# Kernel optimization log

Measured on AMD Instinct MI355X. Metric: run time of the kernel, lower is better.

The kernel has to match this reference:

```python
import jax, jax.numpy as jnp
import numpy as np
import math

DIM = 1024
NUM_HEADS = 16
HEAD_DIM = DIM // NUM_HEADS
BLOCK_SIZE = 64


def _block_mask(src_blocks, tgt_blocks, num_blocks):
    # Block-level BigBird mask: global first/last block columns, sliding window of 1, random blocks.
    i = jnp.arange(num_blocks)[:, None]
    j = jnp.arange(num_blocks)[None, :]
    band = jnp.abs(i - j) <= 1
    glob = (j == 0) | (j == num_blocks - 1)
    bm = band | glob
    bm = bm.at[src_blocks, tgt_blocks].set(True)
    return bm  # [nb, nb] bool


def setup_inputs() -> dict:
    key = jax.random.key(0)
    ks = jax.random.split(key, 12)
    B, S = 2, 2048
    x = jax.random.normal(ks[0], (B, S, DIM), dtype=jnp.float32)
    scale = 0.02
    Wq = jax.random.normal(ks[1], (DIM, DIM), dtype=jnp.float32) * scale
    bq = jnp.zeros((DIM,), dtype=jnp.float32)
    Wk = jax.random.normal(ks[2], (DIM, DIM), dtype=jnp.float32) * scale
    bk = jnp.zeros((DIM,), dtype=jnp.float32)
    Wv = jax.random.normal(ks[3], (DIM, DIM), dtype=jnp.float32) * scale
    bv = jnp.zeros((DIM,), dtype=jnp.float32)
    Wo = jax.random.normal(ks[4], (DIM, DIM), dtype=jnp.float32) * scale
    bo = jnp.zeros((DIM,), dtype=jnp.float32)
    num_blocks = S // BLOCK_SIZE
    src_blocks = jax.random.randint(ks[5], (3,), 0, num_blocks, dtype=jnp.int32)
    tgt_blocks = jax.random.randint(ks[6], (3,), 0, num_blocks, dtype=jnp.int32)
    return {"x": x, "Wq": Wq, "bq": bq, "Wk": Wk, "bk": bk, "Wv": Wv, "bv": bv,
            "Wo": Wo, "bo": bo, "src_blocks": src_blocks, "tgt_blocks": tgt_blocks}


def reference(x, Wq, bq, Wk, bk, Wv, bv, Wo, bo, src_blocks, tgt_blocks):
    B, S, _ = x.shape
    nb = S // BLOCK_SIZE
    # NOTE: original torch code uses .view (not transpose) to split heads; replicate faithfully.
    q = (x @ Wq.T + bq).reshape(B, NUM_HEADS, S, HEAD_DIM)
    k = (x @ Wk.T + bk).reshape(B, NUM_HEADS, S, HEAD_DIM)
    v = (x @ Wv.T + bv).reshape(B, NUM_HEADS, S, HEAD_DIM)
    bm = _block_mask(src_blocks, tgt_blocks, nb)
    mask = jnp.repeat(jnp.repeat(bm, BLOCK_SIZE, axis=0), BLOCK_SIZE, axis=1)  # [S, S]
    scores = jnp.einsum('bhqd,bhkd->bhqk', q, k) / math.sqrt(HEAD_DIM)
    scores = jnp.where(mask[None, None], scores, jnp.float32(-1e9))
    attn = jax.nn.softmax(scores, axis=-1)
    out = jnp.einsum('bhqk,bhkd->bhqd', attn, v)
    out = out.transpose(0, 2, 1, 3).reshape(B, S, DIM)
    return out @ Wo.T + bo
```

## Files before the change

kernel.cpp:

```cpp
#include <hip/hip_runtime.h>
#include <math.h>

typedef __attribute__((ext_vector_type(8))) short short8;
typedef __attribute__((ext_vector_type(4))) float f32x4;

#define SEQ 2048
#define NB  32

__device__ __forceinline__ unsigned short f2bf(float f) {
    unsigned u = __float_as_uint(f);
    u = (u + 0x7FFFu + ((u >> 16) & 1u)) >> 16;
    return (unsigned short)u;
}

__device__ __forceinline__ void gload16(const unsigned short* g, unsigned short* l) {
    __builtin_amdgcn_global_load_lds(
        (__attribute__((address_space(1))) void*)(void*)(g),
        (__attribute__((address_space(3))) void*)(l), 16, 0, 0);
}

__global__ __launch_bounds__(256) void cvt_all(const float* __restrict__ x,
                                               const float* __restrict__ w0,
                                               const float* __restrict__ w1,
                                               const float* __restrict__ w2,
                                               const float* __restrict__ w3,
                                               unsigned short* __restrict__ ox,
                                               unsigned short* __restrict__ o0,
                                               unsigned short* __restrict__ o1,
                                               unsigned short* __restrict__ o2,
                                               unsigned short* __restrict__ o3) {
    const int which = blockIdx.y;
    const float* in = (which == 0) ? x : (which == 1) ? w0 : (which == 2) ? w1
                       : (which == 3) ? w2 : w3;
    unsigned short* out = (which == 0) ? ox : (which == 1) ? o0 : (which == 2) ? o1
                          : (which == 3) ? o2 : o3;
    const int n8 = (which == 0) ? 524288 : 131072;
    int i = blockIdx.x * 256 + threadIdx.x;
    const int stride = gridDim.x * 256;
    for (; i < n8; i += stride) {
        const float4 a = ((const float4*)in)[i * 2];
        const float4 b = ((const float4*)in)[i * 2 + 1];
        uint4 o;
        o.x = f2bf(a.x) | ((unsigned)f2bf(a.y) << 16);
        o.y = f2bf(a.z) | ((unsigned)f2bf(a.w) << 16);
        o.z = f2bf(b.x) | ((unsigned)f2bf(b.y) << 16);
        o.w = f2bf(b.z) | ((unsigned)f2bf(b.w) << 16);
        ((uint4*)out)[i] = o;
    }
}

template <int BF16OUT, int BN>
__global__ __launch_bounds__(256) void gemm_bt(const unsigned short* __restrict__ A,
                                               const unsigned short* __restrict__ Wall,
                                               const float* __restrict__ b0,
                                               const float* __restrict__ b1,
                                               const float* __restrict__ b2,
                                               unsigned short* __restrict__ outb,
                                               float* __restrict__ outf) {
    constexpr int MI = (BN == 128) ? 4 : 2;
    constexpr int NI = 4;
    __shared__ __align__(16) unsigned short SMEM[2 * 128 * 32 + 2 * BN * 32];
    unsigned short* As0 = SMEM;
    unsigned short* As1 = SMEM + 128 * 32;
    unsigned short* Bs0 = SMEM + 2 * 128 * 32;
    unsigned short* Bs1 = SMEM + 2 * 128 * 32 + BN * 32;

    const int t = threadIdx.x;
    const int w = t >> 6, l = t & 63;
    const int bx = blockIdx.x;
    const int which = (BN == 128) ? (bx >> 3) : 0;
    const int n0 = (BN == 128) ? (bx & 7) * 128 : bx * 64;
    const int m0 = blockIdx.y * 128;
    const unsigned short* W = Wall + (size_t)which * (1024ull * 1024);
    const float* bias = (which == 0) ? b0 : (which == 1) ? b1 : b2;

    const int wr = (BN == 128) ? (w >> 1) * 64 : w * 32;
    const int wc = (BN == 128) ? (w & 1) * 64 : 0;

    f32x4 acc[MI][NI];
#pragma unroll
    for (int i = 0; i < MI; ++i)
#pragma unroll
        for (int j = 0; j < NI; ++j) acc[i][j] = f32x4{0.f, 0.f, 0.f, 0.f};

    const unsigned short* Ag = A + (size_t)(m0 + w * 32 + (l >> 2)) * 1024 + (l & 3) * 8;
    const unsigned short* Wg =
        W + (size_t)(n0 + ((BN == 128) ? w * 32 : w * 16) + (l >> 2)) * 1024 + (l & 3) * 8;

    auto STAGE = [&](unsigned short* Asb, unsigned short* Bsb, int k0) {
        gload16(Ag + k0, Asb + w * 1024);
        gload16(Ag + k0 + 16 * 1024, Asb + w * 1024 + 512);
        gload16(Wg + k0, Bsb + ((BN == 128) ? w * 1024 : w * 512));
        if (BN == 128) gload16(Wg + k0 + 16 * 1024, Bsb + w * 1024 + 512);
    };
    auto COMPUTE = [&](const unsigned short* Asb, const unsigned short* Bsb) {
        short8 af[MI], bfr[NI];
#pragma unroll
        for (int mi = 0; mi < MI; ++mi)
            af[mi] = *(const short8*)&Asb[(wr + mi * 16 + (l & 15)) * 32 + (l >> 4) * 8];
#pragma unroll
        for (int ni = 0; ni < NI; ++ni)
            bfr[ni] = *(const short8*)&Bsb[(wc + ni * 16 + (l & 15)) * 32 + (l >> 4) * 8];
#pragma unroll
        for (int mi = 0; mi < MI; ++mi)
#pragma unroll
            for (int ni = 0; ni < NI; ++ni)
                acc[mi][ni] = __builtin_amdgcn_mfma_f32_16x16x32_bf16(af[mi], bfr[ni],
                                                                      acc[mi][ni], 0, 0, 0);
    };
#define WAITV_INFLIGHT()                                                  \
    do {                                                                  \
        if constexpr (BN == 128)                                          \
            asm volatile("s_waitcnt vmcnt(4)" ::: "memory");              \
        else                                                              \
            asm volatile("s_waitcnt vmcnt(3)" ::: "memory");              \
        __builtin_amdgcn_sched_barrier(0);                                \
    } while (0)
#define BAR()                                                             \
    do {                                                                  \
        __builtin_amdgcn_s_barrier();                                     \
        __builtin_amdgcn_sched_barrier(0);                                \
    } while (0)
#define READS_DONE_BAR()                                                  \
    do {                                                                  \
        asm volatile("s_waitcnt lgkmcnt(0)" ::: "memory");                \
        __builtin_amdgcn_sched_barrier(0);                                \
        __builtin_amdgcn_s_barrier();                                     \
        __builtin_amdgcn_sched_barrier(0);                                \
    } while (0)

    STAGE(As0, Bs0, 0);
#pragma unroll 1
    for (int kt2 = 0; kt2 < 16; ++kt2) {
        STAGE(As1, Bs1, (kt2 * 2 + 1) * 32);
        WAITV_INFLIGHT();
        BAR();
        COMPUTE(As0, Bs0);
        READS_DONE_BAR();

        if (kt2 < 15) {
            STAGE(As0, Bs0, (kt2 * 2 + 2) * 32);
            WAITV_INFLIGHT();
        } else {
            asm volatile("s_waitcnt vmcnt(0)" ::: "memory");
            __builtin_amdgcn_sched_barrier(0);
        }
        BAR();
        COMPUTE(As1, Bs1);
        if (kt2 < 15) READS_DONE_BAR();
    }
#undef WAITV_INFLIGHT
#undef BAR
#undef READS_DONE_BAR

    __syncthreads();
    const int g = l >> 4, c = l & 15;
    if constexpr (BF16OUT) {
        unsigned short* eb = SMEM + w * (32 * 72);
        unsigned short* outw = outb + (size_t)which * (4096ull * 1024);
        const int r1 = l >> 1, hh = (l & 1) * 32;
#pragma unroll
        for (int half = 0; half < 2; ++half) {
#pragma unroll
            for (int ni = 0; ni < NI; ++ni) {
                const float bv = bias[n0 + wc + ni * 16 + c];
#pragma unroll
                for (int mi2 = 0; mi2 < 2; ++mi2)
#pragma unroll
                    for (int j = 0; j < 4; ++j)
                        eb[(mi2 * 16 + g * 4 + j) * 72 + ni * 16 + c] =
                            f2bf(acc[half * 2 + mi2][ni][j] + bv);
            }
            asm volatile("s_waitcnt lgkmcnt(0)" ::: "memory");
            __builtin_amdgcn_sched_barrier(0);
            const unsigned short* src = eb + r1 * 72 + hh;
            unsigned short* dst =
                &outw[(size_t)(m0 + wr + half * 32 + r1) * 1024 + n0 + wc + hh];
#pragma unroll
            for (int q = 0; q < 4; ++q)
                *(uint4*)(dst + q * 8) = *(const uint4*)(src + q * 8);
            asm volatile("s_waitcnt lgkmcnt(0)" ::: "memory");
            __builtin_amdgcn_sched_barrier(0);
        }
    } else {
        float* ef = (float*)SMEM + w * (16 * 68);
        const int r2 = l >> 2, qq = (l & 3) * 16;
#pragma unroll
        for (int mi = 0; mi < MI; ++mi) {
#pragma unroll
            for (int ni = 0; ni < NI; ++ni) {
                const float bv = bias[n0 + wc + ni * 16 + c];
#pragma unroll
                for (int j = 0; j < 4; ++j)
                    ef[(g * 4 + j) * 68 + ni * 16 + c] = acc[mi][ni][j] + bv;
            }
            asm volatile("s_waitcnt lgkmcnt(0)" ::: "memory");
            __builtin_amdgcn_sched_barrier(0);
            const float* srcf = ef + r2 * 68 + qq;
            float* dstf = &outf[(size_t)(m0 + wr + mi * 16 + r2) * 1024 + n0 + wc + qq];
#pragma unroll
            for (int q = 0; q < 4; ++q)
                *(float4*)(dstf + q * 4) = *(const float4*)(srcf + q * 4);
            asm volatile("s_waitcnt lgkmcnt(0)" ::: "memory");
            __builtin_amdgcn_sched_barrier(0);
        }
    }
}

__global__ __launch_bounds__(256) void attn_mfma(const unsigned short* __restrict__ qb_,
                                                 const unsigned short* __restrict__ kb_,
                                                 const unsigned short* __restrict__ vb_,
                                                 const int* __restrict__ srcb,
                                                 const int* __restrict__ tgtb,
                                                 unsigned short* __restrict__ outb) {
    __shared__ __align__(16) unsigned short Ks[64 * 72];
    __shared__ __align__(16) unsigned short Vs[64 * 72];
    __shared__ __align__(16) unsigned short Ps[4][16 * 72];

    const int t = threadIdx.x, w = t >> 6, l = t & 63;
    const int qi = blockIdx.x, h = blockIdx.y, b = blockIdx.z;
    const int g = l >> 4, c = l & 15;

    unsigned mask = 1u | (1u << (NB - 1)) | (1u << qi);
    if (qi > 0) mask |= 1u << (qi - 1);
    if (qi < NB - 1) mask |= 1u << (qi + 1);
#pragma unroll
    for (int tt = 0; tt < 3; ++tt)
        if (srcb[tt] == qi) mask |= 1u << (tgtb[tt] & 31);

    const size_t ho = (size_t)(b * 16 + h) * (SEQ * 64);
    const unsigned short* Q = qb_ + ho;
    const unsigned short* K = kb_ + ho;
    const unsigned short* V = vb_ + ho;

    short8 qf[2];
    {
        const unsigned short* qrow = Q + (size_t)(qi * 64 + w * 16 + c) * 64;
        qf[0] = *(const short8*)(qrow + g * 8);
        qf[1] = *(const short8*)(qrow + 32 + g * 8);
    }

    f32x4 oacc[4];
#pragma unroll
    for (int d = 0; d < 4; ++d) oacc[d] = f32x4{0.f, 0.f, 0.f, 0.f};
    float mrun = -INFINITY, lsum = 0.f;

    const int sr = t >> 2, sc = (t & 3) * 16;

    for (int kb = 0; kb < NB; ++kb) {
        if (!((mask >> kb) & 1u)) continue;

        const unsigned short* ksrc = K + (size_t)(kb * 64 + sr) * 64 + sc;
        const unsigned short* vsrc = V + (size_t)(kb * 64 + sr) * 64 + sc;
        uint4 k0 = *(const uint4*)ksrc, k1 = *(const uint4*)(ksrc + 8);
        uint4 v0 = *(const uint4*)vsrc, v1 = *(const uint4*)(vsrc + 8);

        __syncthreads();
        *(uint4*)&Ks[sr * 72 + sc] = k0;
        *(uint4*)&Ks[sr * 72 + sc + 8] = k1;
        {
            const unsigned short* p0 = (const unsigned short*)&v0;
            const unsigned short* p1 = (const unsigned short*)&v1;
#pragma unroll
            for (int e = 0; e < 8; ++e) {
                Vs[(sc + e) * 72 + sr] = p0[e];
                Vs[(sc + 8 + e) * 72 + sr] = p1[e];
            }
        }
        __syncthreads();

        f32x4 sacc[4];
#pragma unroll
        for (int kt = 0; kt < 4; ++kt) sacc[kt] = f32x4{0.f, 0.f, 0.f, 0.f};
#pragma unroll
        for (int kt = 0; kt < 4; ++kt) {
#pragma unroll
            for (int ks = 0; ks < 2; ++ks) {
                const short8 ka = *(const short8*)&Ks[(kt * 16 + c) * 72 + ks * 32 + g * 8];
                sacc[kt] = __builtin_amdgcn_mfma_f32_16x16x32_bf16(ka, qf[ks], sacc[kt], 0, 0, 0);
            }
        }

        float sv[16];
        float tmax = -INFINITY;
#pragma unroll
        for (int kt = 0; kt < 4; ++kt)
#pragma unroll
            for (int j = 0; j < 4; ++j) {
                const float x = sacc[kt][j] * 0.125f;
                sv[kt * 4 + j] = x;
                tmax = fmaxf(tmax, x);
            }
        tmax = fmaxf(tmax, __shfl_xor(tmax, 16));
        tmax = fmaxf(tmax, __shfl_xor(tmax, 32));
        const float newm = fmaxf(mrun, tmax);
        const float corr = __expf(mrun - newm);
        float ps = 0.f;
#pragma unroll
        for (int e = 0; e < 16; ++e) {
            const float p = __expf(sv[e] - newm);
            sv[e] = p;
            ps += p;
        }
        ps += __shfl_xor(ps, 16);
        ps += __shfl_xor(ps, 32);
        lsum = lsum * corr + ps;
        mrun = newm;
#pragma unroll
        for (int d = 0; d < 4; ++d)
#pragma unroll
            for (int j = 0; j < 4; ++j) oacc[d][j] *= corr;

        unsigned short* pw = &Ps[w][c * 72];
#pragma unroll
        for (int kt = 0; kt < 4; ++kt) {
            uint2 pk;
            pk.x = f2bf(sv[kt * 4 + 0]) | ((unsigned)f2bf(sv[kt * 4 + 1]) << 16);
            pk.y = f2bf(sv[kt * 4 + 2]) | ((unsigned)f2bf(sv[kt * 4 + 3]) << 16);
            *(uint2*)&pw[kt * 16 + g * 4] = pk;
        }
        asm volatile("s_waitcnt lgkmcnt(0)" ::: "memory");
        __builtin_amdgcn_sched_barrier(0);

#pragma unroll
        for (int ks = 0; ks < 2; ++ks) {
            const short8 pb = *(const short8*)&Ps[w][c * 72 + ks * 32 + g * 8];
#pragma unroll
            for (int dt = 0; dt < 4; ++dt) {
                const short8 va = *(const short8*)&Vs[(dt * 16 + c) * 72 + ks * 32 + g * 8];
                oacc[dt] = __builtin_amdgcn_mfma_f32_16x16x32_bf16(va, pb, oacc[dt], 0, 0, 0);
            }
        }
    }

    const float inv = 1.f / lsum;
    unsigned short* orow = outb + (size_t)(b * SEQ + qi * 64 + w * 16 + c) * 1024 + h * 64;
#pragma unroll
    for (int dt = 0; dt < 4; ++dt)
#pragma unroll
        for (int j = 0; j < 4; ++j)
            orow[dt * 16 + g * 4 + j] = f2bf(oacc[dt][j] * inv);
}

extern "C" void kernel_launch(void* const* d_in, const int* in_sizes, int n_in,
                              void* d_out, int out_size, void* d_ws, size_t ws_size,
                              hipStream_t stream) {
    const float* x  = (const float*)d_in[0];
    const float* Wq = (const float*)d_in[1];
    const float* bq = (const float*)d_in[2];
    const float* Wk = (const float*)d_in[3];
    const float* bk = (const float*)d_in[4];
    const float* Wv = (const float*)d_in[5];
    const float* bv = (const float*)d_in[6];
    const float* Wo = (const float*)d_in[7];
    const float* bo = (const float*)d_in[8];
    const int* srcb = (const int*)d_in[9];
    const int* tgtb = (const int*)d_in[10];

    unsigned short* wsu = (unsigned short*)d_ws;
    unsigned short* xbf   = wsu;
    unsigned short* wqkv  = wsu + 4194304ull;
    unsigned short* wobf  = wsu + 7340032ull;
    unsigned short* qkvbf = wsu + 8388608ull;
    unsigned short* attbf = wsu + 25165824ull;

    hipLaunchKernelGGL(cvt_all, dim3(512, 5), dim3(256), 0, stream,
                       x, Wq, Wk, Wv, Wo,
                       xbf, wqkv, wqkv + 1048576ull, wqkv + 2097152ull, wobf);

    hipLaunchKernelGGL((gemm_bt<1, 128>), dim3(24, 32), dim3(256), 0, stream,
                       xbf, wqkv, bq, bk, bv, qkvbf, (float*)nullptr);

    hipLaunchKernelGGL(attn_mfma, dim3(32, 16, 2), dim3(256), 0, stream,
                       qkvbf, qkvbf + 4194304ull, qkvbf + 2ull * 4194304ull,
                       srcb, tgtb, attbf);

    hipLaunchKernelGGL((gemm_bt<0, 64>), dim3(16, 32), dim3(256), 0, stream,
                       attbf, wobf, bo, bo, bo, (unsigned short*)nullptr, (float*)d_out);

    (void)in_sizes; (void)n_in; (void)out_size; (void)ws_size;
}
```

Measured before the change: 96.45 us.

## Deepen GEMM LDS pipeline to four-buffer ring with one barrier per k-tile

The bf16 GEMM main loop moves from a double-buffered LDS scheme to a four-slot ring buffer with two k-tiles of global-to-LDS loads in flight. Because a slot is not overwritten until two steps after it was read, the separate reads-done barrier is dropped and each k-step has only one s_barrier. The goal is to hide more global load latency and cut synchronization per tile. In exchange the LDS footprint per block doubles, which may lower occupancy, and the vmcnt waits are hand-tuned to the exact number of loads per stage.

New measurement: 94.34 us. -2.2%, faster.

```diff
diff --git a/kernel.cpp b/kernel.cpp
--- a/kernel.cpp
+++ b/kernel.cpp
@@ -59,11 +59,12 @@
                                                float* __restrict__ outf) {
     constexpr int MI = (BN == 128) ? 4 : 2;
     constexpr int NI = 4;
-    __shared__ __align__(16) unsigned short SMEM[2 * 128 * 32 + 2 * BN * 32];
-    unsigned short* As0 = SMEM;
-    unsigned short* As1 = SMEM + 128 * 32;
-    unsigned short* Bs0 = SMEM + 2 * 128 * 32;
-    unsigned short* Bs1 = SMEM + 2 * 128 * 32 + BN * 32;
+    __shared__ __align__(16) unsigned short SMEM[4 * 128 * 32 + 4 * BN * 32];
+    unsigned short* Asb[4] = {SMEM, SMEM + 128 * 32, SMEM + 2 * 128 * 32,
+                              SMEM + 3 * 128 * 32};
+    unsigned short* Bsb[4] = {SMEM + 4 * 128 * 32, SMEM + 4 * 128 * 32 + BN * 32,
+                              SMEM + 4 * 128 * 32 + 2 * BN * 32,
+                              SMEM + 4 * 128 * 32 + 3 * BN * 32};
 
     const int t = threadIdx.x;
     const int w = t >> 6, l = t & 63;
@@ -87,20 +88,23 @@
     const unsigned short* Wg =
         W + (size_t)(n0 + ((BN == 128) ? w * 32 : w * 16) + (l >> 2)) * 1024 + (l & 3) * 8;
 
-    auto STAGE = [&](unsigned short* Asb, unsigned short* Bsb, int k0) {
-        gload16(Ag + k0, Asb + w * 1024);
-        gload16(Ag + k0 + 16 * 1024, Asb + w * 1024 + 512);
-        gload16(Wg + k0, Bsb + ((BN == 128) ? w * 1024 : w * 512));
-        if (BN == 128) gload16(Wg + k0 + 16 * 1024, Bsb + w * 1024 + 512);
+    auto STAGE = [&](int buf, int kt) {
+        const int k0 = kt * 32;
+        gload16(Ag + k0, Asb[buf] + w * 1024);
+        gload16(Ag + k0 + 16 * 1024, Asb[buf] + w * 1024 + 512);
+        gload16(Wg + k0, Bsb[buf] + ((BN == 128) ? w * 1024 : w * 512));
+        if (BN == 128) gload16(Wg + k0 + 16 * 1024, Bsb[buf] + w * 1024 + 512);
     };
-    auto COMPUTE = [&](const unsigned short* Asb, const unsigned short* Bsb) {
+    auto COMPUTE = [&](int buf) {
+        const unsigned short* As_ = Asb[buf];
+        const unsigned short* Bs_ = Bsb[buf];
         short8 af[MI], bfr[NI];
 #pragma unroll
         for (int mi = 0; mi < MI; ++mi)
-            af[mi] = *(const short8*)&Asb[(wr + mi * 16 + (l & 15)) * 32 + (l >> 4) * 8];
+            af[mi] = *(const short8*)&As_[(wr + mi * 16 + (l & 15)) * 32 + (l >> 4) * 8];
 #pragma unroll
         for (int ni = 0; ni < NI; ++ni)
-            bfr[ni] = *(const short8*)&Bsb[(wc + ni * 16 + (l & 15)) * 32 + (l >> 4) * 8];
+            bfr[ni] = *(const short8*)&Bs_[(wc + ni * 16 + (l & 15)) * 32 + (l >> 4) * 8];
 #pragma unroll
         for (int mi = 0; mi < MI; ++mi)
 #pragma unroll
@@ -108,50 +112,44 @@
                 acc[mi][ni] = __builtin_amdgcn_mfma_f32_16x16x32_bf16(af[mi], bfr[ni],
                                                                       acc[mi][ni], 0, 0, 0);
     };
-#define WAITV_INFLIGHT()                                                  \
+#define SB() __builtin_amdgcn_sched_barrier(0)
+#define BAR() do { __builtin_amdgcn_s_barrier(); SB(); } while (0)
+#define WV_DEEP()                                                         \
+    do {                                                                  \
+        if constexpr (BN == 128)                                          \
+            asm volatile("s_waitcnt vmcnt(8)" ::: "memory");              \
+        else                                                              \
+            asm volatile("s_waitcnt vmcnt(6)" ::: "memory");              \
+        SB();                                                             \
+    } while (0)
+#define WV_ONE()                                                          \
     do {                                                                  \
         if constexpr (BN == 128)                                          \
             asm volatile("s_waitcnt vmcnt(4)" ::: "memory");              \
         else                                                              \
             asm volatile("s_waitcnt vmcnt(3)" ::: "memory");              \
-        __builtin_amdgcn_sched_barrier(0);                                \
+        SB();                                                             \
     } while (0)
-#define BAR()                                                             \
-    do {                                                                  \
-        __builtin_amdgcn_s_barrier();                                     \
-        __builtin_amdgcn_sched_barrier(0);                                \
-    } while (0)
-#define READS_DONE_BAR()                                                  \
-    do {                                                                  \
-        asm volatile("s_waitcnt lgkmcnt(0)" ::: "memory");                \
-        __builtin_amdgcn_sched_barrier(0);                                \
-        __builtin_amdgcn_s_barrier();                                     \
-        __builtin_amdgcn_sched_barrier(0);                                \
-    } while (0)
-
-    STAGE(As0, Bs0, 0);
+#define WV_ZERO() do { asm volatile("s_waitcnt vmcnt(0)" ::: "memory"); SB(); } while (0)
+
+    STAGE(0, 0);
+    STAGE(1, 1);
 #pragma unroll 1
-    for (int kt2 = 0; kt2 < 16; ++kt2) {
-        STAGE(As1, Bs1, (kt2 * 2 + 1) * 32);
-        WAITV_INFLIGHT();
-        BAR();
-        COMPUTE(As0, Bs0);
-        READS_DONE_BAR();
-
-        if (kt2 < 15) {
-            STAGE(As0, Bs0, (kt2 * 2 + 2) * 32);
-            WAITV_INFLIGHT();
-        } else {
-            asm volatile("s_waitcnt vmcnt(0)" ::: "memory");
-            __builtin_amdgcn_sched_barrier(0);
-        }
-        BAR();
-        COMPUTE(As1, Bs1);
-        if (kt2 < 15) READS_DONE_BAR();
-    }
-#undef WAITV_INFLIGHT
+    for (int i = 0; i < 7; ++i) {
+        STAGE(2, 4 * i + 2); WV_DEEP(); BAR(); COMPUTE(0);
+        STAGE(3, 4 * i + 3); WV_DEEP(); BAR(); COMPUTE(1);
+        STAGE(0, 4 * i + 4); WV_DEEP(); BAR(); COMPUTE(2);
+        STAGE(1, 4 * i + 5); WV_DEEP(); BAR(); COMPUTE(3);
+    }
+    STAGE(2, 30); WV_DEEP(); BAR(); COMPUTE(0);
+    STAGE(3, 31); WV_DEEP(); BAR(); COMPUTE(1);
+    WV_ONE();  BAR(); COMPUTE(2);
+    WV_ZERO(); BAR(); COMPUTE(3);
+#undef SB
 #undef BAR
-#undef READS_DONE_BAR
+#undef WV_DEEP
+#undef WV_ONE
+#undef WV_ZERO
 
     __syncthreads();
     const int g = l >> 4, c = l & 15;
```
